# Kernel tuning notes

Measured on AMD Instinct MI355X. Metric: run time of the kernel, lower is better.

Reference implementation:

```python
import jax, jax.numpy as jnp
import numpy as np


def _place(positions, clips):
    """Place each clip into a zero canvas at offset floor(pos * n_samples).

    positions: (B, C) in [0, 1); clips: (B, C, N). Returns (B, C, N) where
    out[b, c, k] = clips[b, c, k - idx] for k >= idx else 0 (no wrap-around).
    """
    n = clips.shape[-1]
    idx = (positions * n).astype(jnp.int32)          # (B, C)
    ar = jnp.arange(n, dtype=jnp.int32)              # (N,)
    src = ar[None, None, :] - idx[:, :, None]        # (B, C, N) source index
    gathered = jnp.take_along_axis(clips, jnp.clip(src, 0, n - 1), axis=-1)
    return jnp.where(src >= 0, gathered, jnp.zeros((), clips.dtype))


def setup_inputs() -> dict:
    key = jax.random.key(0)
    k1, k2, k3 = jax.random.split(key, 3)
    B, C, N = 32, 32, 32768
    x = jax.random.uniform(k1, (B, C), dtype=jnp.float32)
    clips = jax.random.normal(k2, (B, C, N), dtype=jnp.float32)
    actual = jax.random.normal(k3, (B, N), dtype=jnp.float32)
    return {"x": x, "clips": clips, "actual": actual}


def reference(x, clips, actual):
    # RollScheduler.forward -> Position.forward -> position(x, clips, n_samples).
    # `actual` only participates in the custom backward, not the forward value.
    return _place(x, clips)
```

## Files before the change

### kernel.cpp

```cpp
#include <hip/hip_runtime.h>


constexpr int N_SAMPLES = 32768;
constexpr int BLOCK = 256;

__global__ __launch_bounds__(BLOCK) void roll_place_kernel(
    const float* __restrict__ x,
    const float* __restrict__ clips,
    float* __restrict__ out)
{
    const int row = blockIdx.x;
    int idx = (int)(x[row] * (float)N_SAMPLES);
    idx = idx < 0 ? 0 : (idx > N_SAMPLES ? N_SAMPLES : idx);

    const float* __restrict__ src = clips + (size_t)row * N_SAMPLES;
    float* __restrict__ dst = out + (size_t)row * N_SAMPLES;

    const int tid = threadIdx.x;
    constexpr int NV = N_SAMPLES / 4;

    #pragma unroll 4
    for (int v = tid; v < NV; v += BLOCK) {
        const int k0 = v * 4;
        float4 r;
        if (k0 >= idx) {
            const float* p = src + (k0 - idx);
            r.x = p[0];
            r.y = p[1];
            r.z = p[2];
            r.w = p[3];
        } else if (k0 + 3 < idx) {
            r = make_float4(0.f, 0.f, 0.f, 0.f);
        } else {
            float vals[4];
            #pragma unroll
            for (int j = 0; j < 4; ++j) {
                const int k = k0 + j;
                vals[j] = (k >= idx) ? src[k - idx] : 0.f;
            }
            r = make_float4(vals[0], vals[1], vals[2], vals[3]);
        }
        *reinterpret_cast<float4*>(dst + k0) = r;
    }
}

extern "C" void kernel_launch(void* const* d_in, const int* in_sizes, int n_in,
                              void* d_out, int out_size, void* d_ws, size_t ws_size,
                              hipStream_t stream) {
    const float* x     = (const float*)d_in[0];
    const float* clips = (const float*)d_in[1];
    float* out = (float*)d_out;

    const int rows = in_sizes[0];
    roll_place_kernel<<<rows, BLOCK, 0, stream>>>(x, clips, out);
}
```

Measured before the change: 232.0 us.

## Split rows across blocks and use aligned float4 loads with lane shuffling

Each row is now split into four segments handled by separate blocks, so 4096 blocks are launched instead of 1024 to fill more CUs. The per-element scalar loads of the misaligned source are replaced by two aligned float4 loads per output vector, recombined by shifting lanes according to idx mod 4. This aims to raise memory-level parallelism and to vectorise the loads. The cost is reading each source vector twice, though the second read should mostly hit in cache.

New measurement: 234.3 us. Within noise of the previous version (+1.0%).

```diff
diff --git a/kernel.cpp b/kernel.cpp
--- a/kernel.cpp
+++ b/kernel.cpp
@@ -2,45 +2,66 @@
 
 
 constexpr int N_SAMPLES = 32768;
+constexpr int NV = N_SAMPLES / 4;
 constexpr int BLOCK = 256;
+constexpr int SPLIT = 4;
+constexpr int VPB = NV / SPLIT;
 
 __global__ __launch_bounds__(BLOCK) void roll_place_kernel(
     const float* __restrict__ x,
     const float* __restrict__ clips,
     float* __restrict__ out)
 {
-    const int row = blockIdx.x;
+    const int row = blockIdx.x >> 2;
+    const int seg = blockIdx.x & (SPLIT - 1);
+
     int idx = (int)(x[row] * (float)N_SAMPLES);
     idx = idx < 0 ? 0 : (idx > N_SAMPLES ? N_SAMPLES : idx);
+    const int a = idx >> 2;
+    const int r = idx & 3;
 
+    const float4* __restrict__ srcv =
+        reinterpret_cast<const float4*>(clips + (size_t)row * N_SAMPLES);
+    float4* __restrict__ dstv =
+        reinterpret_cast<float4*>(out + (size_t)row * N_SAMPLES);
     const float* __restrict__ src = clips + (size_t)row * N_SAMPLES;
-    float* __restrict__ dst = out + (size_t)row * N_SAMPLES;
 
+    const int v0 = seg * VPB;
+    const int v1 = v0 + VPB;
     const int tid = threadIdx.x;
-    constexpr int NV = N_SAMPLES / 4;
 
-    #pragma unroll 4
-    for (int v = tid; v < NV; v += BLOCK) {
-        const int k0 = v * 4;
-        float4 r;
-        if (k0 >= idx) {
-            const float* p = src + (k0 - idx);
-            r.x = p[0];
-            r.y = p[1];
-            r.z = p[2];
-            r.w = p[3];
-        } else if (k0 + 3 < idx) {
-            r = make_float4(0.f, 0.f, 0.f, 0.f);
-        } else {
-            float vals[4];
-            #pragma unroll
-            for (int j = 0; j < 4; ++j) {
-                const int k = k0 + j;
-                vals[j] = (k >= idx) ? src[k - idx] : 0.f;
+    if (r == 0) {
+        #pragma unroll 4
+        for (int v = v0 + tid; v < v1; v += BLOCK) {
+            float4 o;
+            if (v >= a) {
+                o = srcv[v - a];
+            } else {
+                o = make_float4(0.f, 0.f, 0.f, 0.f);
             }
-            r = make_float4(vals[0], vals[1], vals[2], vals[3]);
+            dstv[v] = o;
         }
-        *reinterpret_cast<float4*>(dst + k0) = r;
+    } else {
+        #pragma unroll 4
+        for (int v = v0 + tid; v < v1; v += BLOCK) {
+            float4 o;
+            if (v > a) {
+                const float4 A  = srcv[v - a - 1];
+                const float4 B4 = srcv[v - a];
+                if (r == 1)      o = make_float4(A.w, B4.x, B4.y, B4.z);
+                else if (r == 2) o = make_float4(A.z, A.w, B4.x, B4.y);
+                else             o = make_float4(A.y, A.z, A.w, B4.x);
+            } else if (v < a) {
+                o = make_float4(0.f, 0.f, 0.f, 0.f);
+            } else {
+                float vals[4];
+                #pragma unroll
+                for (int j = 0; j < 4; ++j)
+                    vals[j] = (j >= r) ? src[j - r] : 0.f;
+                o = make_float4(vals[0], vals[1], vals[2], vals[3]);
+            }
+            dstv[v] = o;
+        }
     }
 }
 
@@ -52,5 +73,5 @@
     float* out = (float*)d_out;
 
     const int rows = in_sizes[0];
-    roll_place_kernel<<<rows, BLOCK, 0, stream>>>(x, clips, out);
+    roll_place_kernel<<<rows * SPLIT, BLOCK, 0, stream>>>(x, clips, out);
 }
```
